# Kernel optimization log

Measured on AMD Instinct MI355X. Metric: run time of the kernel, lower is better.

The kernel has to match this reference:

```python
import jax, jax.numpy as jnp
from jax import lax
import numpy as np

K = 3          # kernel_size
PAD = 1        # K // 2
MAX_OFFSET = 0.1
EPS = 1e-8


def setup_inputs() -> dict:
    key = jax.random.key(0)
    k0, k1, k2 = jax.random.split(key, 3)
    B, C, H, W = 4, 64, 256, 256
    Cmid = C // 4
    x = jax.random.normal(k0, (B, C, H, W), jnp.float32)
    # offset_predictor: Conv2d(C+9, C//4, 3, pad=1) -> LeakyReLU(0.2) -> Conv2d(C//4, 2, 3, pad=1) -> Tanh
    w1 = jax.random.normal(k1, (Cmid, C + K * K, 3, 3), jnp.float32) * 0.05
    b1 = jnp.zeros((Cmid,), jnp.float32)
    w2 = jax.random.normal(k2, (2, Cmid, 3, 3), jnp.float32) * 0.05
    b2 = jnp.zeros((2,), jnp.float32)
    return {"x": x, "w1": w1, "b1": b1, "w2": w2, "b2": b2}


def _conv2d(x, w, b):
    # NCHW, OIHW, stride 1, pad 1 (SAME for 3x3)
    out = lax.conv_general_dilated(x, w, (1, 1), ((PAD, PAD), (PAD, PAD)),
                                   dimension_numbers=("NCHW", "OIHW", "NCHW"))
    return out + b[None, :, None, None]


def _local_cosine_similarity(x):
    # F.unfold with zero padding: neighbors[k] at spatial shift (di-1, dj-1), row-major k = di*K + dj
    B, C, H, W = x.shape
    xp = jnp.pad(x, ((0, 0), (0, 0), (PAD, PAD), (PAD, PAD)))
    neighbors = jnp.stack([xp[:, :, di:di + H, dj:dj + W]
                           for di in range(K) for dj in range(K)], axis=2)  # (B,C,9,H,W)
    center = x[:, :, None, :, :]                                            # (B,C,1,H,W)
    numerator = jnp.sum(neighbors * center, axis=1)                         # (B,9,H,W)
    center_norm = jnp.sqrt(jnp.sum(x * x, axis=1)) + EPS                    # (B,H,W)
    neighbor_norm = jnp.sqrt(jnp.sum(neighbors * neighbors, axis=1)) + EPS  # (B,9,H,W)
    return numerator / (center_norm[:, None] * neighbor_norm)               # (B,9,H,W)


def _grid_sample_border(x, grid):
    # bilinear, padding_mode='border', align_corners=True; grid: (B,H,W,2) with (gx,gy) in [-1,1]
    B, C, H, W = x.shape
    ix = (grid[..., 0] + 1.0) * 0.5 * (W - 1)
    iy = (grid[..., 1] + 1.0) * 0.5 * (H - 1)
    ix = jnp.clip(ix, 0.0, W - 1)
    iy = jnp.clip(iy, 0.0, H - 1)
    x0f = jnp.floor(ix); y0f = jnp.floor(iy)
    wx = ix - x0f; wy = iy - y0f
    x0 = x0f.astype(jnp.int32); y0 = y0f.astype(jnp.int32)
    x1 = jnp.minimum(x0 + 1, W - 1); y1 = jnp.minimum(y0 + 1, H - 1)

    def gather(img, yy, xx):  # img (C,H,W), yy/xx (H,W) -> (C,H,W)
        return img[:, yy, xx]

    g = jax.vmap(gather)
    v00 = g(x, y0, x0); v01 = g(x, y0, x1)
    v10 = g(x, y1, x0); v11 = g(x, y1, x1)
    wx = wx[:, None]; wy = wy[:, None]  # broadcast over channel dim
    return ((1 - wy) * ((1 - wx) * v00 + wx * v01)
            + wy * ((1 - wx) * v10 + wx * v11))


def reference(x, w1, b1, w2, b2):
    B, C, H, W = x.shape
    sim = _local_cosine_similarity(x)                       # (B,9,H,W)
    features = jnp.concatenate([x, sim], axis=1)            # (B,C+9,H,W)
    h = _conv2d(features, w1, b1)
    h = jnp.where(h >= 0, h, 0.2 * h)                       # LeakyReLU(0.2)
    offset = jnp.tanh(_conv2d(h, w2, b2)) * MAX_OFFSET      # (B,2,H,W)
    gy, gx = jnp.meshgrid(jnp.linspace(-1.0, 1.0, H),
                          jnp.linspace(-1.0, 1.0, W), indexing="ij")
    base_grid = jnp.stack([gx, gy], axis=-1)[None]          # (1,H,W,2)
    offset_grid = base_grid + jnp.transpose(offset, (0, 2, 3, 1))
    return _grid_sample_border(x, offset_grid)
```

## Files before the change

kernel.cpp:

```cpp
#include <hip/hip_runtime.h>
#include <math.h>

#define B 4
#define C 64
#define H 256
#define W 256
#define CMID 16
#define CIN 73
#define HW (H*W)
#define NW (CIN*9*CMID)
#define XS_STRIDE 260

__global__ void transpose_w1_kernel(const float* __restrict__ w1, float* __restrict__ wt) {
    int tid = blockIdx.x * blockDim.x + threadIdx.x;
    if (tid >= NW) return;
    int co = tid & (CMID - 1);
    int rest = tid >> 4;
    int ci = rest / 9;
    int k = rest - ci * 9;
    wt[tid] = w1[(co * CIN + ci) * 9 + k];
}

__device__ __forceinline__ void read_patch_lds(const float* __restrict__ xsbuf,
                                               int rl, int px, float v[3][4]) {
    const float* pb = xsbuf + rl * XS_STRIDE + px;
#pragma unroll
    for (int r = 0; r < 3; ++r) {
        float2 p0 = *(const float2*)(pb + r * XS_STRIDE);
        float2 p1 = *(const float2*)(pb + r * XS_STRIDE + 2);
        v[r][0] = p0.x; v[r][1] = p0.y; v[r][2] = p1.x; v[r][3] = p1.y;
    }
}

__global__ __launch_bounds__(256) void sim_kernel(const float* __restrict__ x,
                                                  float* __restrict__ sim) {
    __shared__ float xs[2][4 * XS_STRIDE];
    int bid = blockIdx.x;
    int b  = bid >> 7;
    int y0 = (bid & 127) << 1;
    int tid = threadIdx.x;
    int srow = tid >> 6;
    int sx4  = (tid & 63) << 2;
    int rl = tid >> 7;
    int px = (tid & 127) << 1;
    int y  = y0 + rl;

    int grow = y0 - 1 + srow;
    bool gvalid = (grow >= 0) && (grow < H);
    const float* gsrc = x + (size_t)b * C * HW + (size_t)grow * W + sx4;

    if (tid < 16) {
        int bu = tid >> 3, r = (tid >> 1) & 3, e = (tid & 1) ? 257 : 0;
        xs[bu][r * XS_STRIDE + e] = 0.f;
    }

    float dot0[9], dot1[9], nsq0[9], nsq1[9];
    float csq0 = 0.f, csq1 = 0.f;
#pragma unroll
    for (int i = 0; i < 9; ++i) { dot0[i] = dot1[i] = nsq0[i] = nsq1[i] = 0.f; }

    float4 r4 = make_float4(0.f, 0.f, 0.f, 0.f);
    if (gvalid) r4 = *(const float4*)gsrc;

    int cur = 0;
#pragma unroll 1
    for (int ci = 0; ci < C; ++ci) {
        float* dst = &xs[cur][srow * XS_STRIDE + 1 + sx4];
        dst[0] = r4.x; dst[1] = r4.y; dst[2] = r4.z; dst[3] = r4.w;
        __syncthreads();
        if (ci + 1 < C) {
            r4 = make_float4(0.f, 0.f, 0.f, 0.f);
            if (gvalid) r4 = *(const float4*)(gsrc + (size_t)(ci + 1) * HW);
        }
        float v[3][4];
        read_patch_lds(xs[cur], rl, px, v);
        float cv0 = v[1][1], cv1 = v[1][2];
        csq0 = fmaf(cv0, cv0, csq0);
        csq1 = fmaf(cv1, cv1, csq1);
#pragma unroll
        for (int kr = 0; kr < 3; ++kr)
#pragma unroll
            for (int kc = 0; kc < 3; ++kc) {
                int kk = kr * 3 + kc;
                if (kk == 4) continue;
                float n0 = v[kr][kc], n1 = v[kr][kc + 1];
                dot0[kk] = fmaf(cv0, n0, dot0[kk]);
                nsq0[kk] = fmaf(n0, n0, nsq0[kk]);
                dot1[kk] = fmaf(cv1, n1, dot1[kk]);
                nsq1[kk] = fmaf(n1, n1, nsq1[kk]);
            }
        cur ^= 1;
    }
    dot0[4] = csq0; nsq0[4] = csq0;
    dot1[4] = csq1; nsq1[4] = csq1;

    float cn0 = sqrtf(csq0) + 1e-8f;
    float cn1 = sqrtf(csq1) + 1e-8f;
    float* so = sim + (size_t)b * 9 * HW + (size_t)y * W + px;
#pragma unroll
    for (int kk = 0; kk < 9; ++kk) {
        float s0 = dot0[kk] / (cn0 * (sqrtf(nsq0[kk]) + 1e-8f));
        float s1 = dot1[kk] / (cn1 * (sqrtf(nsq1[kk]) + 1e-8f));
        *(float2*)(so + (size_t)kk * HW) = make_float2(s0, s1);
    }
}

__device__ __forceinline__ void conv1_chan(const float* __restrict__ xsbuf,
                                           int rl, int px,
                                           const float* __restrict__ wp,
                                           float acc0[CMID], float acc1[CMID]) {
    float v[3][4];
    read_patch_lds(xsbuf, rl, px, v);
#pragma unroll
    for (int kr = 0; kr < 3; ++kr)
#pragma unroll
        for (int kc = 0; kc < 3; ++kc) {
            float a0 = v[kr][kc], a1 = v[kr][kc + 1];
            const float* w = wp + (kr * 3 + kc) * CMID;
#pragma unroll
            for (int co = 0; co < CMID; ++co) {
                float wv = w[co];
                acc0[co] = fmaf(a0, wv, acc0[co]);
                acc1[co] = fmaf(a1, wv, acc1[co]);
            }
        }
}

__global__ __launch_bounds__(256) void conv1_kernel(const float* __restrict__ x,
                                                    const float* __restrict__ sim,
                                                    const float* __restrict__ wt,
                                                    const float* __restrict__ b1,
                                                    float* __restrict__ h) {
    __shared__ float xs[2][2][4 * XS_STRIDE];

    int tid = threadIdx.x;
    int bid = blockIdx.x;
    int b  = bid >> 7;
    int y0 = (bid & 127) << 1;
    int srow = tid >> 6;
    int sx4  = (tid & 63) << 2;
    int rl = tid >> 7;
    int px = (tid & 127) << 1;
    int y  = y0 + rl;

    int grow = y0 - 1 + srow;
    bool gvalid = (grow >= 0) && (grow < H);
    const float* gx = x   + (size_t)b * C * HW + (size_t)grow * W + sx4;
    const float* gs = sim + (size_t)b * 9 * HW + (size_t)grow * W + sx4;

    if (tid < 32) {
        int bu = tid >> 4, ch = (tid >> 3) & 1, r = (tid >> 1) & 3;
        int e = (tid & 1) ? 257 : 0;
        xs[bu][ch][r * XS_STRIDE + e] = 0.f;
    }

    float acc0[CMID], acc1[CMID];
#pragma unroll
    for (int co = 0; co < CMID; ++co) { acc0[co] = b1[co]; acc1[co] = b1[co]; }

    float4 p0 = make_float4(0.f, 0.f, 0.f, 0.f), p1 = p0;
    if (gvalid) {
        p0 = *(const float4*)gx;
        p1 = *(const float4*)(gx + HW);
    }

    int cur = 0;
#pragma unroll 1
    for (int cc = 0; cc < CIN; cc += 2) {
        float* d0 = &xs[cur][0][srow * XS_STRIDE + 1 + sx4];
        float* d1 = &xs[cur][1][srow * XS_STRIDE + 1 + sx4];
        d0[0] = p0.x; d0[1] = p0.y; d0[2] = p0.z; d0[3] = p0.w;
        d1[0] = p1.x; d1[1] = p1.y; d1[2] = p1.z; d1[3] = p1.w;
        __syncthreads();

        if (cc + 2 < CIN && gvalid) {
            int ci = cc + 2;
            p0 = (ci < C) ? *(const float4*)(gx + (size_t)ci * HW)
                          : *(const float4*)(gs + (size_t)(ci - C) * HW);
        }
        if (cc + 3 < CIN && gvalid) {
            int ci = cc + 3;
            p1 = (ci < C) ? *(const float4*)(gx + (size_t)ci * HW)
                          : *(const float4*)(gs + (size_t)(ci - C) * HW);
        }

        conv1_chan(xs[cur][0], rl, px, wt + cc * 144, acc0, acc1);
        if (cc + 1 < CIN)
            conv1_chan(xs[cur][1], rl, px, wt + (cc + 1) * 144, acc0, acc1);
        cur ^= 1;
    }

    float* ho = h + (size_t)b * CMID * HW + (size_t)y * W + px;
#pragma unroll
    for (int co = 0; co < CMID; ++co) {
        float v0 = acc0[co], v1 = acc1[co];
        v0 = v0 >= 0.f ? v0 : 0.2f * v0;
        v1 = v1 >= 0.f ? v1 : 0.2f * v1;
        *(float2*)(ho + (size_t)co * HW) = make_float2(v0, v1);
    }
}

__global__ __launch_bounds__(256) void offset_kernel(const float* __restrict__ h,
                                                     const float* __restrict__ w2,
                                                     const float* __restrict__ b2,
                                                     float2* __restrict__ off_buf) {
    __shared__ float lw2[CMID * 9 * 2];
    __shared__ float xs[2][4 * XS_STRIDE];

    int tid = threadIdx.x;
    for (int i = tid; i < CMID * 9 * 2; i += 256) {
        int co = i & 1;
        int rest = i >> 1;
        int ci = rest / 9;
        int kk = rest - ci * 9;
        lw2[i] = w2[(co * CMID + ci) * 9 + kk];
    }

    int bid = blockIdx.x;
    int b  = bid >> 7;
    int y0 = (bid & 127) << 1;
    int srow = tid >> 6;
    int sx4  = (tid & 63) << 2;
    int rl = tid >> 7;
    int px = (tid & 127) << 1;
    int y  = y0 + rl;

    int grow = y0 - 1 + srow;
    bool gvalid = (grow >= 0) && (grow < H);
    const float* gh = h + (size_t)b * CMID * HW + (size_t)grow * W + sx4;

    if (tid < 16) {
        int bu = tid >> 3, r = (tid >> 1) & 3, e = (tid & 1) ? 257 : 0;
        xs[bu][r * XS_STRIDE + e] = 0.f;
    }

    float s0x = b2[0], s0y = b2[1], s1x = b2[0], s1y = b2[1];

    float4 r4 = make_float4(0.f, 0.f, 0.f, 0.f);
    if (gvalid) r4 = *(const float4*)gh;

    int cur = 0;
#pragma unroll 1
    for (int ci = 0; ci < CMID; ++ci) {
        float* dst = &xs[cur][srow * XS_STRIDE + 1 + sx4];
        dst[0] = r4.x; dst[1] = r4.y; dst[2] = r4.z; dst[3] = r4.w;
        __syncthreads();
        if (ci + 1 < CMID) {
            r4 = make_float4(0.f, 0.f, 0.f, 0.f);
            if (gvalid) r4 = *(const float4*)(gh + (size_t)(ci + 1) * HW);
        }
        float v[3][4];
        read_patch_lds(xs[cur], rl, px, v);
#pragma unroll
        for (int kr = 0; kr < 3; ++kr)
#pragma unroll
            for (int kc = 0; kc < 3; ++kc) {
                float2 wv = *(const float2*)(lw2 + (ci * 9 + kr * 3 + kc) * 2);
                s0x = fmaf(v[kr][kc],     wv.x, s0x);
                s0y = fmaf(v[kr][kc],     wv.y, s0y);
                s1x = fmaf(v[kr][kc + 1], wv.x, s1x);
                s1y = fmaf(v[kr][kc + 1], wv.y, s1y);
            }
        cur ^= 1;
    }

    float ix0 = (float)px       + 0.1f * tanhf(s0x) * (0.5f * (float)(W - 1));
    float iy0 = (float)y        + 0.1f * tanhf(s0y) * (0.5f * (float)(H - 1));
    float ix1 = (float)(px + 1) + 0.1f * tanhf(s1x) * (0.5f * (float)(W - 1));
    float iy1 = (float)y        + 0.1f * tanhf(s1y) * (0.5f * (float)(H - 1));
    ix0 = fminf(fmaxf(ix0, 0.f), (float)(W - 1));
    iy0 = fminf(fmaxf(iy0, 0.f), (float)(H - 1));
    ix1 = fminf(fmaxf(ix1, 0.f), (float)(W - 1));
    iy1 = fminf(fmaxf(iy1, 0.f), (float)(H - 1));

    float4* op = (float4*)(off_buf + (size_t)b * HW + (size_t)y * W + px);
    *op = make_float4(ix0, iy0, ix1, iy1);
}

#define SROWS 35
__global__ __launch_bounds__(256) void sample_kernel(const float* __restrict__ x,
                                                     const float2* __restrict__ off_buf,
                                                     float* __restrict__ out) {
    __shared__ float xs[SROWS * 256];

    int bid = blockIdx.x;
    int sb = (bid & 7) * 16 + (bid >> 3);
    int b  = sb >> 5;
    int ty = sb & 31;
    int cg = blockIdx.y;
    int tid = threadIdx.x;

    int ybase = ty << 3;
    int lo = ybase - 13;

    int a00[8], a01[8], a10[8], a11[8];
    float wx[8], wy[8];
    const float2* ob2 = off_buf + (size_t)b * HW + (size_t)ybase * W + tid;
#pragma unroll
    for (int r = 0; r < 8; ++r) {
        float2 o = ob2[r * W];
        float xf = floorf(o.x), yf = floorf(o.y);
        wx[r] = o.x - xf; wy[r] = o.y - yf;
        int x0 = (int)xf, yy0 = (int)yf;
        int x1 = min(x0 + 1, W - 1), yy1 = min(yy0 + 1, H - 1);
        int r0 = (yy0 - lo) << 8, r1 = (yy1 - lo) << 8;
        a00[r] = r0 + x0; a01[r] = r0 + x1;
        a10[r] = r1 + x0; a11[r] = r1 + x1;
    }

    const float* xb = x + ((size_t)b * C + cg * 4) * HW;
    float* outb = out + ((size_t)b * C + cg * 4) * HW + (size_t)ybase * W + tid;

#pragma unroll 1
    for (int c = 0; c < 4; ++c) {
        __syncthreads();
        const float* src = xb + (size_t)c * HW;
        for (int j = tid; j < SROWS * 64; j += 256) {
            int row = j >> 6, x4 = (j & 63) << 2;
            int grw = min(max(lo + row, 0), H - 1);
            *(float4*)&xs[(row << 8) + x4] = *(const float4*)(src + (size_t)grw * W + x4);
        }
        __syncthreads();
        float* oc = outb + (size_t)c * HW;
#pragma unroll
        for (int r = 0; r < 8; ++r) {
            float v00 = xs[a00[r]], v01 = xs[a01[r]];
            float v10 = xs[a10[r]], v11 = xs[a11[r]];
            float top = fmaf(wx[r], v01 - v00, v00);
            float bot = fmaf(wx[r], v11 - v10, v10);
            oc[r * W] = fmaf(wy[r], bot - top, top);
        }
    }
}

extern "C" void kernel_launch(void* const* d_in, const int* in_sizes, int n_in,
                              void* d_out, int out_size, void* d_ws, size_t ws_size,
                              hipStream_t stream) {
    const float* x  = (const float*)d_in[0];
    const float* w1 = (const float*)d_in[1];
    const float* b1 = (const float*)d_in[2];
    const float* w2 = (const float*)d_in[3];
    const float* b2 = (const float*)d_in[4];
    float* out = (float*)d_out;

    float* ws  = (float*)d_ws;
    float* wt  = ws;
    float* sim = ws + 16384;
    float* h   = sim + (size_t)B * 9 * HW;
    float2* off_buf = (float2*)(h + (size_t)B * CMID * HW);

    transpose_w1_kernel<<<(NW + 255) / 256, 256, 0, stream>>>(w1, wt);

    sim_kernel<<<512, 256, 0, stream>>>(x, sim);
    conv1_kernel<<<512, 256, 0, stream>>>(x, sim, wt, b1, h);
    offset_kernel<<<512, 256, 0, stream>>>(h, w2, b2, off_buf);
    sample_kernel<<<dim3(128, 16), 256, 0, stream>>>(x, off_buf, out);
}
```

Measured before the change: 263.4 us.

## Remap sim and conv1 to one output row per block, four channels per sync

The sim and conv1 kernels now assign one output row per 256-thread block (one pixel per thread) instead of two rows with two pixels per thread, doubling the grid to B*H blocks. Each stage loads four channels of a 3-row halo into LDS per barrier rather than one or two, so there are fewer __syncthreads calls and more loads in flight. This halves the per-thread accumulator count (more occupancy) but triples the global rows loaded per output row instead of 4 rows per 2, increasing global/L2 traffic and weight reads per pixel.

```diff
diff --git a/kernel.cpp b/kernel.cpp
--- a/kernel.cpp
+++ b/kernel.cpp
@@ -21,109 +21,115 @@
     wt[tid] = w1[(co * CIN + ci) * 9 + k];
 }
 
-__device__ __forceinline__ void read_patch_lds(const float* __restrict__ xsbuf,
-                                               int rl, int px, float v[3][4]) {
-    const float* pb = xsbuf + rl * XS_STRIDE + px;
+
+__device__ __forceinline__ void read_patch9(const float* __restrict__ base, float v[9]) {
 #pragma unroll
     for (int r = 0; r < 3; ++r) {
-        float2 p0 = *(const float2*)(pb + r * XS_STRIDE);
-        float2 p1 = *(const float2*)(pb + r * XS_STRIDE + 2);
-        v[r][0] = p0.x; v[r][1] = p0.y; v[r][2] = p1.x; v[r][3] = p1.y;
+        v[r * 3 + 0] = base[r * XS_STRIDE + 0];
+        v[r * 3 + 1] = base[r * XS_STRIDE + 1];
+        v[r * 3 + 2] = base[r * XS_STRIDE + 2];
+    }
+}
+
+__device__ __forceinline__ void zero_halo48(float* __restrict__ xs0, int tid) {
+    if (tid < 48) {
+        int e = tid & 1;
+        int r = (tid >> 1) % 3;
+        int q = (tid >> 1) / 3;
+        xs0[q * (3 * XS_STRIDE) + r * XS_STRIDE + (e ? 257 : 0)] = 0.f;
     }
 }
 
 __global__ __launch_bounds__(256) void sim_kernel(const float* __restrict__ x,
                                                   float* __restrict__ sim) {
-    __shared__ float xs[2][4 * XS_STRIDE];
+    __shared__ float xs[2][4][3 * XS_STRIDE];
+
     int bid = blockIdx.x;
-    int b  = bid >> 7;
-    int y0 = (bid & 127) << 1;
+    int b = bid >> 8;
+    int y = bid & 255;
     int tid = threadIdx.x;
-    int srow = tid >> 6;
-    int sx4  = (tid & 63) << 2;
-    int rl = tid >> 7;
-    int px = (tid & 127) << 1;
-    int y  = y0 + rl;
-
-    int grow = y0 - 1 + srow;
-    bool gvalid = (grow >= 0) && (grow < H);
-    const float* gsrc = x + (size_t)b * C * HW + (size_t)grow * W + sx4;
-
-    if (tid < 16) {
-        int bu = tid >> 3, r = (tid >> 1) & 3, e = (tid & 1) ? 257 : 0;
-        xs[bu][r * XS_STRIDE + e] = 0.f;
-    }
-
-    float dot0[9], dot1[9], nsq0[9], nsq1[9];
-    float csq0 = 0.f, csq1 = 0.f;
-#pragma unroll
-    for (int i = 0; i < 9; ++i) { dot0[i] = dot1[i] = nsq0[i] = nsq1[i] = 0.f; }
-
-    float4 r4 = make_float4(0.f, 0.f, 0.f, 0.f);
-    if (gvalid) r4 = *(const float4*)gsrc;
+
+    const float* xb = x + (size_t)b * C * HW;
+
+    bool rv[3];
+    long off[3];
+#pragma unroll
+    for (int j = 0; j < 3; ++j) {
+        int grow = y - 1 + j;
+        rv[j] = (grow >= 0) && (grow < H);
+        off[j] = (long)grow * W + tid;
+    }
+
+    zero_halo48(&xs[0][0][0], tid);
+
+    float dot[9], nsq[9];
+    float csq = 0.f;
+#pragma unroll
+    for (int i = 0; i < 9; ++i) { dot[i] = nsq[i] = 0.f; }
+
+    float p[12];
+#pragma unroll
+    for (int k = 0; k < 4; ++k)
+#pragma unroll
+        for (int j = 0; j < 3; ++j)
+            p[k * 3 + j] = rv[j] ? xb[(size_t)k * HW + off[j]] : 0.f;
 
     int cur = 0;
 #pragma unroll 1
-    for (int ci = 0; ci < C; ++ci) {
-        float* dst = &xs[cur][srow * XS_STRIDE + 1 + sx4];
-        dst[0] = r4.x; dst[1] = r4.y; dst[2] = r4.z; dst[3] = r4.w;
-        __syncthreads();
-        if (ci + 1 < C) {
-            r4 = make_float4(0.f, 0.f, 0.f, 0.f);
-            if (gvalid) r4 = *(const float4*)(gsrc + (size_t)(ci + 1) * HW);
-        }
-        float v[3][4];
-        read_patch_lds(xs[cur], rl, px, v);
-        float cv0 = v[1][1], cv1 = v[1][2];
-        csq0 = fmaf(cv0, cv0, csq0);
-        csq1 = fmaf(cv1, cv1, csq1);
-#pragma unroll
-        for (int kr = 0; kr < 3; ++kr)
-#pragma unroll
-            for (int kc = 0; kc < 3; ++kc) {
-                int kk = kr * 3 + kc;
+    for (int cc = 0; cc < C; cc += 4) {
+#pragma unroll
+        for (int k = 0; k < 4; ++k)
+#pragma unroll
+            for (int j = 0; j < 3; ++j)
+                xs[cur][k][j * XS_STRIDE + 1 + tid] = p[k * 3 + j];
+        __syncthreads();
+
+        if (cc + 4 < C) {
+#pragma unroll
+            for (int k = 0; k < 4; ++k)
+#pragma unroll
+                for (int j = 0; j < 3; ++j)
+                    p[k * 3 + j] = rv[j] ? xb[(size_t)(cc + 4 + k) * HW + off[j]] : 0.f;
+        }
+
+#pragma unroll
+        for (int k = 0; k < 4; ++k) {
+            float v[9];
+            read_patch9(&xs[cur][k][tid], v);
+            float cv = v[4];
+            csq = fmaf(cv, cv, csq);
+#pragma unroll
+            for (int kk = 0; kk < 9; ++kk) {
                 if (kk == 4) continue;
-                float n0 = v[kr][kc], n1 = v[kr][kc + 1];
-                dot0[kk] = fmaf(cv0, n0, dot0[kk]);
-                nsq0[kk] = fmaf(n0, n0, nsq0[kk]);
-                dot1[kk] = fmaf(cv1, n1, dot1[kk]);
-                nsq1[kk] = fmaf(n1, n1, nsq1[kk]);
+                dot[kk] = fmaf(cv, v[kk], dot[kk]);
+                nsq[kk] = fmaf(v[kk], v[kk], nsq[kk]);
             }
+        }
         cur ^= 1;
     }
-    dot0[4] = csq0; nsq0[4] = csq0;
-    dot1[4] = csq1; nsq1[4] = csq1;
-
-    float cn0 = sqrtf(csq0) + 1e-8f;
-    float cn1 = sqrtf(csq1) + 1e-8f;
-    float* so = sim + (size_t)b * 9 * HW + (size_t)y * W + px;
-#pragma unroll
-    for (int kk = 0; kk < 9; ++kk) {
-        float s0 = dot0[kk] / (cn0 * (sqrtf(nsq0[kk]) + 1e-8f));
-        float s1 = dot1[kk] / (cn1 * (sqrtf(nsq1[kk]) + 1e-8f));
-        *(float2*)(so + (size_t)kk * HW) = make_float2(s0, s1);
-    }
-}
-
-__device__ __forceinline__ void conv1_chan(const float* __restrict__ xsbuf,
-                                           int rl, int px,
-                                           const float* __restrict__ wp,
-                                           float acc0[CMID], float acc1[CMID]) {
-    float v[3][4];
-    read_patch_lds(xsbuf, rl, px, v);
-#pragma unroll
-    for (int kr = 0; kr < 3; ++kr)
-#pragma unroll
-        for (int kc = 0; kc < 3; ++kc) {
-            float a0 = v[kr][kc], a1 = v[kr][kc + 1];
-            const float* w = wp + (kr * 3 + kc) * CMID;
-#pragma unroll
-            for (int co = 0; co < CMID; ++co) {
-                float wv = w[co];
-                acc0[co] = fmaf(a0, wv, acc0[co]);
-                acc1[co] = fmaf(a1, wv, acc1[co]);
-            }
-        }
+
+    dot[4] = csq;
+    nsq[4] = csq;
+    float cn = sqrtf(csq) + 1e-8f;
+    float* so = sim + (size_t)b * 9 * HW + (size_t)y * W + tid;
+#pragma unroll
+    for (int kk = 0; kk < 9; ++kk)
+        so[(size_t)kk * HW] = dot[kk] / (cn * (sqrtf(nsq[kk]) + 1e-8f));
+}
+
+__device__ __forceinline__ void conv1_chan1(const float* __restrict__ base,
+                                            const float* __restrict__ wp,
+                                            float acc[CMID]) {
+    float v[9];
+    read_patch9(base, v);
+#pragma unroll
+    for (int k = 0; k < 9; ++k) {
+        const float* w = wp + k * CMID;
+        float a = v[k];
+#pragma unroll
+        for (int co = 0; co < CMID; ++co)
+            acc[co] = fmaf(a, w[co], acc[co]);
+    }
 }
 
 __global__ __launch_bounds__(256) void conv1_kernel(const float* __restrict__ x,
@@ -131,72 +137,90 @@
                                                     const float* __restrict__ wt,
                                                     const float* __restrict__ b1,
                                                     float* __restrict__ h) {
-    __shared__ float xs[2][2][4 * XS_STRIDE];
-
+    __shared__ float xs[2][4][3 * XS_STRIDE];
+
+    int bid = blockIdx.x;
+    int b = bid >> 8;
+    int y = bid & 255;
     int tid = threadIdx.x;
-    int bid = blockIdx.x;
-    int b  = bid >> 7;
-    int y0 = (bid & 127) << 1;
-    int srow = tid >> 6;
-    int sx4  = (tid & 63) << 2;
-    int rl = tid >> 7;
-    int px = (tid & 127) << 1;
-    int y  = y0 + rl;
-
-    int grow = y0 - 1 + srow;
-    bool gvalid = (grow >= 0) && (grow < H);
-    const float* gx = x   + (size_t)b * C * HW + (size_t)grow * W + sx4;
-    const float* gs = sim + (size_t)b * 9 * HW + (size_t)grow * W + sx4;
-
-    if (tid < 32) {
-        int bu = tid >> 4, ch = (tid >> 3) & 1, r = (tid >> 1) & 3;
-        int e = (tid & 1) ? 257 : 0;
-        xs[bu][ch][r * XS_STRIDE + e] = 0.f;
-    }
-
-    float acc0[CMID], acc1[CMID];
-#pragma unroll
-    for (int co = 0; co < CMID; ++co) { acc0[co] = b1[co]; acc1[co] = b1[co]; }
-
-    float4 p0 = make_float4(0.f, 0.f, 0.f, 0.f), p1 = p0;
-    if (gvalid) {
-        p0 = *(const float4*)gx;
-        p1 = *(const float4*)(gx + HW);
-    }
+
+    const float* gx = x + (size_t)b * C * HW;
+    const float* gs = sim + (size_t)b * 9 * HW;
+
+    bool rv[3];
+    long off[3];
+#pragma unroll
+    for (int j = 0; j < 3; ++j) {
+        int grow = y - 1 + j;
+        rv[j] = (grow >= 0) && (grow < H);
+        off[j] = (long)grow * W + tid;
+    }
+
+    zero_halo48(&xs[0][0][0], tid);
+
+    float acc[CMID];
+#pragma unroll
+    for (int co = 0; co < CMID; ++co) acc[co] = b1[co];
+
+    float p[12];
+#pragma unroll
+    for (int k = 0; k < 4; ++k)
+#pragma unroll
+        for (int j = 0; j < 3; ++j)
+            p[k * 3 + j] = rv[j] ? gx[(size_t)k * HW + off[j]] : 0.f;
 
     int cur = 0;
 #pragma unroll 1
-    for (int cc = 0; cc < CIN; cc += 2) {
-        float* d0 = &xs[cur][0][srow * XS_STRIDE + 1 + sx4];
-        float* d1 = &xs[cur][1][srow * XS_STRIDE + 1 + sx4];
-        d0[0] = p0.x; d0[1] = p0.y; d0[2] = p0.z; d0[3] = p0.w;
-        d1[0] = p1.x; d1[1] = p1.y; d1[2] = p1.z; d1[3] = p1.w;
-        __syncthreads();
-
-        if (cc + 2 < CIN && gvalid) {
-            int ci = cc + 2;
-            p0 = (ci < C) ? *(const float4*)(gx + (size_t)ci * HW)
-                          : *(const float4*)(gs + (size_t)(ci - C) * HW);
-        }
-        if (cc + 3 < CIN && gvalid) {
-            int ci = cc + 3;
-            p1 = (ci < C) ? *(const float4*)(gx + (size_t)ci * HW)
-                          : *(const float4*)(gs + (size_t)(ci - C) * HW);
-        }
-
-        conv1_chan(xs[cur][0], rl, px, wt + cc * 144, acc0, acc1);
-        if (cc + 1 < CIN)
-            conv1_chan(xs[cur][1], rl, px, wt + (cc + 1) * 144, acc0, acc1);
+    for (int cc = 0; cc < 72; cc += 4) {
+#pragma unroll
+        for (int k = 0; k < 4; ++k)
+#pragma unroll
+            for (int j = 0; j < 3; ++j)
+                xs[cur][k][j * XS_STRIDE + 1 + tid] = p[k * 3 + j];
+        __syncthreads();
+
+#pragma unroll
+        for (int k = 0; k < 4; ++k) {
+            int ci = cc + 4 + k;
+            if (ci < CIN) {
+                const float* cb = (ci < C) ? (gx + (size_t)ci * HW)
+                                           : (gs + (size_t)(ci - C) * HW);
+#pragma unroll
+                for (int j = 0; j < 3; ++j)
+                    p[k * 3 + j] = rv[j] ? cb[off[j]] : 0.f;
+            }
+        }
+
+        conv1_chan1(&xs[cur][0][tid], wt + (size_t)cc * 144, acc);
+        conv1_chan1(&xs[cur][1][tid], wt + (size_t)(cc + 1) * 144, acc);
+        conv1_chan1(&xs[cur][2][tid], wt + (size_t)(cc + 2) * 144, acc);
+        conv1_chan1(&xs[cur][3][tid], wt + (size_t)(cc + 3) * 144, acc);
         cur ^= 1;
     }
 
-    float* ho = h + (size_t)b * CMID * HW + (size_t)y * W + px;
+#pragma unroll
+    for (int j = 0; j < 3; ++j)
+        xs[cur][0][j * XS_STRIDE + 1 + tid] = p[j];
+    __syncthreads();
+    conv1_chan1(&xs[cur][0][tid], wt + (size_t)72 * 144, acc);
+
+    float* ho = h + (size_t)b * CMID * HW + (size_t)y * W + tid;
 #pragma unroll
     for (int co = 0; co < CMID; ++co) {
-        float v0 = acc0[co], v1 = acc1[co];
+        float v0 = acc[co];
         v0 = v0 >= 0.f ? v0 : 0.2f * v0;
-        v1 = v1 >= 0.f ? v1 : 0.2f * v1;
-        *(float2*)(ho + (size_t)co * HW) = make_float2(v0, v1);
+        ho[(size_t)co * HW] = v0;
+    }
+}
+
+__device__ __forceinline__ void read_patch_lds(const float* __restrict__ xsbuf,
+                                               int rl, int px, float v[3][4]) {
+    const float* pb = xsbuf + rl * XS_STRIDE + px;
+#pragma unroll
+    for (int r = 0; r < 3; ++r) {
+        float2 p0 = *(const float2*)(pb + r * XS_STRIDE);
+        float2 p1 = *(const float2*)(pb + r * XS_STRIDE + 2);
+        v[r][0] = p0.x; v[r][1] = p0.y; v[r][2] = p1.x; v[r][3] = p1.y;
     }
 }
 
@@ -351,8 +375,8 @@
 
     transpose_w1_kernel<<<(NW + 255) / 256, 256, 0, stream>>>(w1, wt);
 
-    sim_kernel<<<512, 256, 0, stream>>>(x, sim);
-    conv1_kernel<<<512, 256, 0, stream>>>(x, sim, wt, b1, h);
+    sim_kernel<<<B * H, 256, 0, stream>>>(x, sim);
+    conv1_kernel<<<B * H, 256, 0, stream>>>(x, sim, wt, b1, h);
     offset_kernel<<<512, 256, 0, stream>>>(h, w2, b2, off_buf);
     sample_kernel<<<dim3(128, 16), 256, 0, stream>>>(x, off_buf, out);
 }
```

Result: faster. 256.6 us (-2.6%).
